# Kernel tuning notes

Measured on AMD Instinct MI355X. Metric: run time of the kernel, lower is better.

The kernel has to match this reference:

```python
import jax, jax.numpy as jnp
import numpy as np

ALPHA = 0.95   # membrane leak factor exp(-dt/tau_mem)
RHO   = 0.98   # threshold-adaptation decay
BETA  = 1.8    # adaptive threshold gain (ALIF)
TH0   = 1.0    # base threshold
SCALE = 10.0   # SuperSpike surrogate slope

@jax.custom_vjp
def spike(v):
    # Heaviside spike with SuperSpike surrogate gradient (as in cantata's SurrGradSpike)
    return (v >= 0.0).astype(v.dtype)

def _spike_fwd(v):
    return spike(v), v

def _spike_bwd(v, g):
    return (g / (SCALE * jnp.abs(v) + 1.0) ** 2,)

spike.defvjp(_spike_fwd, _spike_bwd)

def _onehot_delays(k, n, d):
    # each presynaptic source is routed through exactly one delay bin
    idx = jax.random.randint(k, (n,), 0, d)
    return (jnp.arange(d)[:, None] == idx[None, :]).astype(jnp.float32)  # [d, n]

def setup_inputs() -> dict:
    B, N, D, NE, DE = 32, 4096, 8, 2048, 4
    key = jax.random.key(0)
    ks = jax.random.split(key, 8)
    V = jax.random.normal(ks[0], (B, N), jnp.float32)
    a = jax.random.uniform(ks[1], (B, N), jnp.float32)
    Xd = (jax.random.uniform(ks[2], (D, B, N)) < 0.05).astype(jnp.float32)      # internal delay ring buffer
    Xext = (jax.random.uniform(ks[3], (DE, B, NE)) < 0.05).astype(jnp.float32)  # delayed external spikes
    W_int = jax.random.normal(ks[4], (N, N), jnp.float32) * 0.02
    W_ext = jax.random.normal(ks[5], (NE, N), jnp.float32) * 0.02
    dmap_int = _onehot_delays(ks[6], N, D)
    dmap_ext = _onehot_delays(ks[7], NE, DE)
    return dict(V=V, a=a, Xd=Xd, Xext=Xext, W_int=W_int, W_ext=W_ext,
                dmap_int=dmap_int, dmap_ext=dmap_ext)

def reference(V, a, Xd, Xext, W_int, W_ext, dmap_int, dmap_ext):
    # 1) ALIF spike generation from membrane + adaptive threshold
    th = TH0 + BETA * a
    X = spike(V - th)                                     # [B,N]
    a_new = RHO * a + X
    # 2) push new spikes into the delay ring buffer (delay 0 = current step)
    Xd_new = jnp.concatenate([X[None], Xd[:-1]], axis=0)  # [D,B,N]
    # 3) delay-mapped synaptic current: gather each presyn source from its delay bin,
    #    then dense delta-synapse accumulation (internal + cross-area)
    x_int = jnp.einsum('dbi,di->bi', Xd_new, dmap_int)    # [B,N]
    x_ext = jnp.einsum('dbi,di->bi', Xext, dmap_ext)      # [B,NE]
    current = x_int @ W_int + x_ext @ W_ext               # [B,N]
    # 4) membrane update: leak, reset on spike, integrate current
    V_new = ALPHA * V * (1.0 - X) + current
    return jnp.stack([X, V_new, a_new])                   # [3,B,N]
```

## Files before the change

### kernel.cpp

```cpp
#include <hip/hip_runtime.h>


#define B_   32
#define N_   4096
#define D_   8
#define NE_  2048
#define DE_  4
#define BN_  (B_ * N_)
#define BNE_ (B_ * NE_)
#define NCHI 64
#define NCHE 32

__device__ __forceinline__ float4 ld4(const float* p) { return *(const float4*)p; }
__device__ __forceinline__ void add4(float4& a, const float4 w) {
    a.x += w.x; a.y += w.y; a.z += w.z; a.w += w.w;
}

__global__ __launch_bounds__(256) void snn_spike_compact(
    const float* __restrict__ V, const float* __restrict__ a,
    const float* __restrict__ Xd, const float* __restrict__ Xext,
    const float* __restrict__ dmap_int, const float* __restrict__ dmap_ext,
    float* __restrict__ out,
    int* __restrict__ cnt_int, int* __restrict__ cnt_ext,
    unsigned short* __restrict__ list_int, unsigned short* __restrict__ list_ext)
{
#pragma clang fp contract(off)
    int tid = threadIdx.x;
    int lane = tid & 63;
    int o = tid >> 6;
    int c = blockIdx.x;
    if (c < NCHI) {
        int i = c * 64 + lane;
        int di = 0;
        #pragma unroll
        for (int d = 1; d < D_; ++d)
            if (dmap_int[d * N_ + i] != 0.0f) di = d;
        unsigned m = 0;
        #pragma unroll
        for (int bb = 0; bb < 8; ++bb) {
            int b = o * 8 + bb;
            int t = b * N_ + i;
            float av = a[t];
            float vv = V[t];
            float th = 1.0f + 1.8f * av;
            float x = (vv - th >= 0.0f) ? 1.0f : 0.0f;
            out[t] = x;
            out[2 * BN_ + t] = 0.98f * av + x;
            float xi = (di == 0) ? x : Xd[(size_t)(di - 1) * BN_ + t];
            if (xi != 0.0f) m |= 1u << bb;
        }
        #pragma unroll
        for (int bb = 0; bb < 8; ++bb) {
            int b = o * 8 + bb;
            unsigned long long bal = __ballot((m >> bb) & 1u);
            int pos = __popcll(bal & ((1ull << lane) - 1ull));
            if ((m >> bb) & 1u) list_int[b * N_ + c * 64 + pos] = (unsigned short)i;
            if (lane == 0) cnt_int[b * NCHI + c] = (int)__popcll(bal);
        }
    } else {
        int cc = c - NCHI;
        int j = cc * 64 + lane;
        int de = 0;
        #pragma unroll
        for (int d = 1; d < DE_; ++d)
            if (dmap_ext[d * NE_ + j] != 0.0f) de = d;
        unsigned m = 0;
        #pragma unroll
        for (int bb = 0; bb < 8; ++bb) {
            int b = o * 8 + bb;
            float xe = Xext[(size_t)de * BNE_ + b * NE_ + j];
            if (xe != 0.0f) m |= 1u << bb;
        }
        #pragma unroll
        for (int bb = 0; bb < 8; ++bb) {
            int b = o * 8 + bb;
            unsigned long long bal = __ballot((m >> bb) & 1u);
            int pos = __popcll(bal & ((1ull << lane) - 1ull));
            if ((m >> bb) & 1u) list_ext[b * NE_ + cc * 64 + pos] = (unsigned short)j;
            if (lane == 0) cnt_ext[b * NCHE + cc] = (int)__popcll(bal);
        }
    }
}

__device__ __forceinline__ void accum_rows(const float* __restrict__ W,
                                           const unsigned short* sl, int n, int j,
                                           float4& acc)
{
    if (n <= 0) return;
    int nf = n & ~7;
    if (nf >= 8) {
        uint4 g = *(const uint4*)(sl);
        float4 p0 = ld4(W + (size_t)(g.x & 0xffff) * N_ + j);
        float4 p1 = ld4(W + (size_t)(g.x >> 16)    * N_ + j);
        float4 p2 = ld4(W + (size_t)(g.y & 0xffff) * N_ + j);
        float4 p3 = ld4(W + (size_t)(g.y >> 16)    * N_ + j);
        float4 p4 = ld4(W + (size_t)(g.z & 0xffff) * N_ + j);
        float4 p5 = ld4(W + (size_t)(g.z >> 16)    * N_ + j);
        float4 p6 = ld4(W + (size_t)(g.w & 0xffff) * N_ + j);
        float4 p7 = ld4(W + (size_t)(g.w >> 16)    * N_ + j);
        for (int k = 8; k < nf; k += 8) {
            uint4 g2 = *(const uint4*)(sl + k);
            float4 q0 = ld4(W + (size_t)(g2.x & 0xffff) * N_ + j);
            float4 q1 = ld4(W + (size_t)(g2.x >> 16)    * N_ + j);
            float4 q2 = ld4(W + (size_t)(g2.y & 0xffff) * N_ + j);
            float4 q3 = ld4(W + (size_t)(g2.y >> 16)    * N_ + j);
            float4 q4 = ld4(W + (size_t)(g2.z & 0xffff) * N_ + j);
            float4 q5 = ld4(W + (size_t)(g2.z >> 16)    * N_ + j);
            float4 q6 = ld4(W + (size_t)(g2.w & 0xffff) * N_ + j);
            float4 q7 = ld4(W + (size_t)(g2.w >> 16)    * N_ + j);
            add4(acc, p0); add4(acc, p1); add4(acc, p2); add4(acc, p3);
            add4(acc, p4); add4(acc, p5); add4(acc, p6); add4(acc, p7);
            p0 = q0; p1 = q1; p2 = q2; p3 = q3;
            p4 = q4; p5 = q5; p6 = q6; p7 = q7;
        }
        add4(acc, p0); add4(acc, p1); add4(acc, p2); add4(acc, p3);
        add4(acc, p4); add4(acc, p5); add4(acc, p6); add4(acc, p7);
    }
    for (int k = nf; k < n; ++k) {
        float4 w = ld4(W + (size_t)sl[k] * N_ + j);
        add4(acc, w);
    }
}

__global__ __launch_bounds__(256, 2) void snn_current(
    const float* __restrict__ W_int, const float* __restrict__ W_ext,
    const float* __restrict__ V, float* __restrict__ out,
    const int* __restrict__ cnt_int, const int* __restrict__ cnt_ext,
    const unsigned short* __restrict__ list_int,
    const unsigned short* __restrict__ list_ext)
{
    __shared__ __align__(16) unsigned short s_int[N_];
    __shared__ __align__(16) unsigned short s_ext[NE_];
    __shared__ int s_oi[NCHI + 1], s_oe[NCHE + 1];
    __shared__ float4 s_red[4][64];

    int tid = threadIdx.x;
    int w = tid >> 6, lane = tid & 63;
    int tile = blockIdx.x;
    int b = blockIdx.y;

    if (tid == 0) {
        int s = 0; s_oi[0] = 0;
        for (int c = 0; c < NCHI; ++c) { s += cnt_int[b * NCHI + c]; s_oi[c + 1] = s; }
    } else if (tid == 64) {
        int s = 0; s_oe[0] = 0;
        for (int c = 0; c < NCHE; ++c) { s += cnt_ext[b * NCHE + c]; s_oe[c + 1] = s; }
    }
    __syncthreads();
    #pragma unroll
    for (int r = 0; r < (NCHI * 64) / 256; ++r) {
        int idx = r * 256 + tid;
        int c = idx >> 6, ss = idx & 63;
        int base = s_oi[c];
        if (ss < s_oi[c + 1] - base) s_int[base + ss] = list_int[b * N_ + idx];
    }
    #pragma unroll
    for (int r = 0; r < (NCHE * 64) / 256; ++r) {
        int idx = r * 256 + tid;
        int c = idx >> 6, ss = idx & 63;
        int base = s_oe[c];
        if (ss < s_oe[c + 1] - base) s_ext[base + ss] = list_ext[b * NE_ + idx];
    }
    __syncthreads();
    int ni = s_oi[NCHI], ne = s_oe[NCHE];

    int j = tile * 256 + lane * 4;
    float4 acc = make_float4(0.f, 0.f, 0.f, 0.f);

    int qi = ((ni + 31) >> 5) << 3;
    int si = w * qi;
    accum_rows(W_int, s_int + si, min(ni, si + qi) - si, j, acc);
    int qe = ((ne + 31) >> 5) << 3;
    int se = w * qe;
    accum_rows(W_ext, s_ext + se, min(ne, se + qe) - se, j, acc);

    s_red[w][lane] = acc;
    __syncthreads();
    if (w == 0) {
        float4 a0 = s_red[0][lane], a1 = s_red[1][lane];
        float4 a2 = s_red[2][lane], a3 = s_red[3][lane];
        float4 cur;
        cur.x = (a0.x + a1.x) + (a2.x + a3.x);
        cur.y = (a0.y + a1.y) + (a2.y + a3.y);
        cur.z = (a0.z + a1.z) + (a2.z + a3.z);
        cur.w = (a0.w + a1.w) + (a2.w + a3.w);
        int t = b * N_ + j;
        float4 v = ld4(V + t);
        float4 x = ld4(out + t);
        float4 vn;
        vn.x = 0.95f * v.x * (1.0f - x.x) + cur.x;
        vn.y = 0.95f * v.y * (1.0f - x.y) + cur.y;
        vn.z = 0.95f * v.z * (1.0f - x.z) + cur.z;
        vn.w = 0.95f * v.w * (1.0f - x.w) + cur.w;
        *(float4*)(out + BN_ + t) = vn;
    }
}

extern "C" void kernel_launch(void* const* d_in, const int* in_sizes, int n_in,
                              void* d_out, int out_size, void* d_ws, size_t ws_size,
                              hipStream_t stream)
{
    const float* V        = (const float*)d_in[0];
    const float* a        = (const float*)d_in[1];
    const float* Xd       = (const float*)d_in[2];
    const float* Xext     = (const float*)d_in[3];
    const float* W_int    = (const float*)d_in[4];
    const float* W_ext    = (const float*)d_in[5];
    const float* dmap_int = (const float*)d_in[6];
    const float* dmap_ext = (const float*)d_in[7];
    float* out = (float*)d_out;

    int*            cnt_int  = (int*)d_ws;
    int*            cnt_ext  = (int*)((char*)d_ws + 8192);
    unsigned short* list_int = (unsigned short*)((char*)d_ws + 12288);
    unsigned short* list_ext = (unsigned short*)((char*)d_ws + 274432);

    snn_spike_compact<<<NCHI + NCHE, 256, 0, stream>>>(
        V, a, Xd, Xext, dmap_int, dmap_ext, out,
        cnt_int, cnt_ext, list_int, list_ext);

    dim3 g2(16, B_);
    snn_current<<<g2, 256, 0, stream>>>(
        W_int, W_ext, V, out, cnt_int, cnt_ext, list_int, list_ext);
}
```

Before: 152.2 us.

## Precompute merged interleaved spike lists in separate kernel and use scalar row indices

Adds a merge kernel that builds, once per batch row, a compacted spike-index list interleaved across the four waves. Each of the 512 current blocks then just bulk-copies its list instead of redoing the prefix scan and scatter. Row indices pass through readfirstlane so the compiler can treat them as wave-uniform scalar addresses. The cost is an extra kernel launch and a third serial stage, and the launch-bounds occupancy hint of 2 is dropped.

```diff
diff --git a/kernel.cpp b/kernel.cpp
--- a/kernel.cpp
+++ b/kernel.cpp
@@ -10,11 +10,14 @@
 #define BNE_ (B_ * NE_)
 #define NCHI 64
 #define NCHE 32
+#define MI_STRIDE 4096
+#define ME_STRIDE 2048
 
 __device__ __forceinline__ float4 ld4(const float* p) { return *(const float4*)p; }
 __device__ __forceinline__ void add4(float4& a, const float4 w) {
     a.x += w.x; a.y += w.y; a.z += w.z; a.w += w.w;
 }
+__device__ __forceinline__ int qalign(int n) { return (((n + 3) >> 2) + 7) & ~7; }
 
 __global__ __launch_bounds__(256) void snn_spike_compact(
     const float* __restrict__ V, const float* __restrict__ a,
@@ -82,6 +85,38 @@
     }
 }
 
+__global__ __launch_bounds__(256) void snn_merge(
+    const int* __restrict__ cnt_int, const int* __restrict__ cnt_ext,
+    const unsigned short* __restrict__ list_int,
+    const unsigned short* __restrict__ list_ext,
+    unsigned short* __restrict__ mint, unsigned short* __restrict__ mext,
+    int* __restrict__ hdr)
+{
+    __shared__ int s_pi[NCHI + 1], s_pe[NCHE + 1];
+    int tid = threadIdx.x, b = blockIdx.x;
+    if (tid < NCHI) s_pi[tid + 1] = cnt_int[b * NCHI + tid];
+    if (tid >= 64 && tid < 64 + NCHE) s_pe[tid - 63] = cnt_ext[b * NCHE + (tid - 64)];
+    __syncthreads();
+    if (tid == 0) { s_pi[0] = 0; for (int c = 0; c < NCHI; ++c) s_pi[c + 1] += s_pi[c]; }
+    else if (tid == 64) { s_pe[0] = 0; for (int c = 0; c < NCHE; ++c) s_pe[c + 1] += s_pe[c]; }
+    __syncthreads();
+    int ni = s_pi[NCHI], ne = s_pe[NCHE];
+    int Qi = qalign(ni), Qe = qalign(ne);
+    for (int e = tid; e < ni; e += 256) {
+        int lo = 0, hi = NCHI;
+        while (hi - lo > 1) { int mid = (lo + hi) >> 1; if (s_pi[mid] <= e) lo = mid; else hi = mid; }
+        unsigned short r = list_int[b * N_ + lo * 64 + (e - s_pi[lo])];
+        mint[b * MI_STRIDE + (e & 3) * Qi + (e >> 2)] = r;
+    }
+    for (int e = tid; e < ne; e += 256) {
+        int lo = 0, hi = NCHE;
+        while (hi - lo > 1) { int mid = (lo + hi) >> 1; if (s_pe[mid] <= e) lo = mid; else hi = mid; }
+        unsigned short r = list_ext[b * NE_ + lo * 64 + (e - s_pe[lo])];
+        mext[b * ME_STRIDE + (e & 3) * Qe + (e >> 2)] = r;
+    }
+    if (tid == 0) { hdr[b * 2] = ni; hdr[b * 2 + 1] = ne; }
+}
+
 __device__ __forceinline__ void accum_rows(const float* __restrict__ W,
                                            const unsigned short* sl, int n, int j,
                                            float4& acc)
@@ -90,24 +125,32 @@
     int nf = n & ~7;
     if (nf >= 8) {
         uint4 g = *(const uint4*)(sl);
-        float4 p0 = ld4(W + (size_t)(g.x & 0xffff) * N_ + j);
-        float4 p1 = ld4(W + (size_t)(g.x >> 16)    * N_ + j);
-        float4 p2 = ld4(W + (size_t)(g.y & 0xffff) * N_ + j);
-        float4 p3 = ld4(W + (size_t)(g.y >> 16)    * N_ + j);
-        float4 p4 = ld4(W + (size_t)(g.z & 0xffff) * N_ + j);
-        float4 p5 = ld4(W + (size_t)(g.z >> 16)    * N_ + j);
-        float4 p6 = ld4(W + (size_t)(g.w & 0xffff) * N_ + j);
-        float4 p7 = ld4(W + (size_t)(g.w >> 16)    * N_ + j);
+        unsigned gx = __builtin_amdgcn_readfirstlane(g.x);
+        unsigned gy = __builtin_amdgcn_readfirstlane(g.y);
+        unsigned gz = __builtin_amdgcn_readfirstlane(g.z);
+        unsigned gw = __builtin_amdgcn_readfirstlane(g.w);
+        float4 p0 = ld4(W + (size_t)(gx & 0xffff) * N_ + j);
+        float4 p1 = ld4(W + (size_t)(gx >> 16)    * N_ + j);
+        float4 p2 = ld4(W + (size_t)(gy & 0xffff) * N_ + j);
+        float4 p3 = ld4(W + (size_t)(gy >> 16)    * N_ + j);
+        float4 p4 = ld4(W + (size_t)(gz & 0xffff) * N_ + j);
+        float4 p5 = ld4(W + (size_t)(gz >> 16)    * N_ + j);
+        float4 p6 = ld4(W + (size_t)(gw & 0xffff) * N_ + j);
+        float4 p7 = ld4(W + (size_t)(gw >> 16)    * N_ + j);
         for (int k = 8; k < nf; k += 8) {
             uint4 g2 = *(const uint4*)(sl + k);
-            float4 q0 = ld4(W + (size_t)(g2.x & 0xffff) * N_ + j);
-            float4 q1 = ld4(W + (size_t)(g2.x >> 16)    * N_ + j);
-            float4 q2 = ld4(W + (size_t)(g2.y & 0xffff) * N_ + j);
-            float4 q3 = ld4(W + (size_t)(g2.y >> 16)    * N_ + j);
-            float4 q4 = ld4(W + (size_t)(g2.z & 0xffff) * N_ + j);
-            float4 q5 = ld4(W + (size_t)(g2.z >> 16)    * N_ + j);
-            float4 q6 = ld4(W + (size_t)(g2.w & 0xffff) * N_ + j);
-            float4 q7 = ld4(W + (size_t)(g2.w >> 16)    * N_ + j);
+            unsigned hx = __builtin_amdgcn_readfirstlane(g2.x);
+            unsigned hy = __builtin_amdgcn_readfirstlane(g2.y);
+            unsigned hz = __builtin_amdgcn_readfirstlane(g2.z);
+            unsigned hw = __builtin_amdgcn_readfirstlane(g2.w);
+            float4 q0 = ld4(W + (size_t)(hx & 0xffff) * N_ + j);
+            float4 q1 = ld4(W + (size_t)(hx >> 16)    * N_ + j);
+            float4 q2 = ld4(W + (size_t)(hy & 0xffff) * N_ + j);
+            float4 q3 = ld4(W + (size_t)(hy >> 16)    * N_ + j);
+            float4 q4 = ld4(W + (size_t)(hz & 0xffff) * N_ + j);
+            float4 q5 = ld4(W + (size_t)(hz >> 16)    * N_ + j);
+            float4 q6 = ld4(W + (size_t)(hw & 0xffff) * N_ + j);
+            float4 q7 = ld4(W + (size_t)(hw >> 16)    * N_ + j);
             add4(acc, p0); add4(acc, p1); add4(acc, p2); add4(acc, p3);
             add4(acc, p4); add4(acc, p5); add4(acc, p6); add4(acc, p7);
             p0 = q0; p1 = q1; p2 = q2; p3 = q3;
@@ -117,21 +160,21 @@
         add4(acc, p4); add4(acc, p5); add4(acc, p6); add4(acc, p7);
     }
     for (int k = nf; k < n; ++k) {
-        float4 w = ld4(W + (size_t)sl[k] * N_ + j);
+        unsigned r = __builtin_amdgcn_readfirstlane((unsigned)sl[k]);
+        float4 w = ld4(W + (size_t)r * N_ + j);
         add4(acc, w);
     }
 }
 
-__global__ __launch_bounds__(256, 2) void snn_current(
+__global__ __launch_bounds__(256) void snn_current(
     const float* __restrict__ W_int, const float* __restrict__ W_ext,
     const float* __restrict__ V, float* __restrict__ out,
-    const int* __restrict__ cnt_int, const int* __restrict__ cnt_ext,
-    const unsigned short* __restrict__ list_int,
-    const unsigned short* __restrict__ list_ext)
-{
-    __shared__ __align__(16) unsigned short s_int[N_];
-    __shared__ __align__(16) unsigned short s_ext[NE_];
-    __shared__ int s_oi[NCHI + 1], s_oe[NCHE + 1];
+    const unsigned short* __restrict__ mint,
+    const unsigned short* __restrict__ mext,
+    const int* __restrict__ hdr)
+{
+    __shared__ __align__(16) unsigned short s_int[MI_STRIDE];
+    __shared__ __align__(16) unsigned short s_ext[ME_STRIDE];
     __shared__ float4 s_red[4][64];
 
     int tid = threadIdx.x;
@@ -139,40 +182,23 @@
     int tile = blockIdx.x;
     int b = blockIdx.y;
 
-    if (tid == 0) {
-        int s = 0; s_oi[0] = 0;
-        for (int c = 0; c < NCHI; ++c) { s += cnt_int[b * NCHI + c]; s_oi[c + 1] = s; }
-    } else if (tid == 64) {
-        int s = 0; s_oe[0] = 0;
-        for (int c = 0; c < NCHE; ++c) { s += cnt_ext[b * NCHE + c]; s_oe[c + 1] = s; }
-    }
-    __syncthreads();
-    #pragma unroll
-    for (int r = 0; r < (NCHI * 64) / 256; ++r) {
-        int idx = r * 256 + tid;
-        int c = idx >> 6, ss = idx & 63;
-        int base = s_oi[c];
-        if (ss < s_oi[c + 1] - base) s_int[base + ss] = list_int[b * N_ + idx];
-    }
-    #pragma unroll
-    for (int r = 0; r < (NCHE * 64) / 256; ++r) {
-        int idx = r * 256 + tid;
-        int c = idx >> 6, ss = idx & 63;
-        int base = s_oe[c];
-        if (ss < s_oe[c + 1] - base) s_ext[base + ss] = list_ext[b * NE_ + idx];
-    }
-    __syncthreads();
-    int ni = s_oi[NCHI], ne = s_oe[NCHE];
+    int ni = hdr[b * 2], ne = hdr[b * 2 + 1];
+    int Qi = qalign(ni), Qe = qalign(ne);
+    int n4i = (4 * Qi) >> 3;
+    const uint4* gi = (const uint4*)(mint + b * MI_STRIDE);
+    for (int k = tid; k < n4i; k += 256) ((uint4*)s_int)[k] = gi[k];
+    int n4e = (4 * Qe) >> 3;
+    const uint4* ge = (const uint4*)(mext + b * ME_STRIDE);
+    for (int k = tid; k < n4e; k += 256) ((uint4*)s_ext)[k] = ge[k];
+    __syncthreads();
 
     int j = tile * 256 + lane * 4;
     float4 acc = make_float4(0.f, 0.f, 0.f, 0.f);
 
-    int qi = ((ni + 31) >> 5) << 3;
-    int si = w * qi;
-    accum_rows(W_int, s_int + si, min(ni, si + qi) - si, j, acc);
-    int qe = ((ne + 31) >> 5) << 3;
-    int se = w * qe;
-    accum_rows(W_ext, s_ext + se, min(ne, se + qe) - se, j, acc);
+    int di = ni - w; int nwi = di > 0 ? (di + 3) >> 2 : 0;
+    accum_rows(W_int, s_int + w * Qi, nwi, j, acc);
+    int de = ne - w; int nwe = de > 0 ? (de + 3) >> 2 : 0;
+    accum_rows(W_ext, s_ext + w * Qe, nwe, j, acc);
 
     s_red[w][lane] = acc;
     __syncthreads();
@@ -214,12 +240,18 @@
     int*            cnt_ext  = (int*)((char*)d_ws + 8192);
     unsigned short* list_int = (unsigned short*)((char*)d_ws + 12288);
     unsigned short* list_ext = (unsigned short*)((char*)d_ws + 274432);
+    unsigned short* mint     = (unsigned short*)((char*)d_ws + 405504);
+    unsigned short* mext     = (unsigned short*)((char*)d_ws + 667648);
+    int*            hdr      = (int*)((char*)d_ws + 798720);
 
     snn_spike_compact<<<NCHI + NCHE, 256, 0, stream>>>(
         V, a, Xd, Xext, dmap_int, dmap_ext, out,
         cnt_int, cnt_ext, list_int, list_ext);
 
+    snn_merge<<<B_, 256, 0, stream>>>(
+        cnt_int, cnt_ext, list_int, list_ext, mint, mext, hdr);
+
     dim3 g2(16, B_);
     snn_current<<<g2, 256, 0, stream>>>(
-        W_int, W_ext, V, out, cnt_int, cnt_ext, list_int, list_ext);
-}
+        W_int, W_ext, V, out, mint, mext, hdr);
+}
```

Measured after the change: 151.0 us. Within noise of the previous version (-0.8%).
